# Optimization experiments

Hardware: AMD Instinct MI355X
Metric: run time of the kernel (lower is better)

The kernel has to match this reference:

```python
import jax, jax.numpy as jnp
import numpy as np

N_USERS, N_ITEMS = 3000, 3000
N = N_USERS + N_ITEMS
E = 100000
DIMS = [(N, 32), (32, 64), (64, 64), (64, 32)]  # RGCN layer (in,out) dims
NUM_REL = 2


def setup_inputs():
    key = jax.random.key(0)
    ks = iter(jax.random.split(key, 40))
    def p(shape, s=0.05):
        return jax.random.normal(next(ks), shape, dtype=jnp.float32) * s
    inp = {}
    for l, (i, o) in enumerate(DIMS):
        inp[f'basis{l}'] = p((4, i, o))      # basis matrices
        inp[f'comp{l}'] = p((NUM_REL, 4), 0.5)  # per-relation basis coefficients
        inp[f'root{l}'] = p((i, o))          # root/self weight
        inp[f'rbias{l}'] = jnp.zeros((o,), jnp.float32)
    inp['gat_w'] = p((32, 512))
    inp['gat_att_src'] = p((512,))
    inp['gat_att_dst'] = p((512,))
    inp['gat_bias'] = jnp.zeros((512,), jnp.float32)
    inp['w1'] = p((1024, 128))
    inp['b1'] = jnp.zeros((128,), jnp.float32)
    inp['w2'] = p((128, 1))
    inp['b2'] = jnp.zeros((1,), jnp.float32)
    inp['edge_index'] = jax.random.randint(next(ks), (2, E), 0, N)
    inp['edge_type'] = jax.random.randint(next(ks), (E,), 0, NUM_REL)
    return inp


def rgcn_layer(x, src, dst, edge_type, basis, comp, root, bias):
    # basis-decomposed relation weights: W[r] = sum_b comp[r,b] * basis[b]
    W = jnp.einsum('rb,bio->rio', comp, basis)  # [R, in, out]
    out = x @ root + bias                        # root/self term
    for r in range(NUM_REL):                     # fixed small relation count
        hr = x @ W[r]                            # [N, out]
        mask = (edge_type == r).astype(x.dtype)  # [E]
        msg = hr[src] * mask[:, None]            # gather + relation mask
        s = jax.ops.segment_sum(msg, dst, num_segments=N)
        cnt = jax.ops.segment_sum(mask, dst, num_segments=N)
        out = out + s / jnp.maximum(cnt, 1.0)[:, None]  # mean aggregation
    return out


def gat_layer(x, src, dst, w, a_src, a_dst, bias):
    # GATConv (1 head, negative_slope=0.2) with self-loops added (PyG default)
    loop = jnp.arange(N)
    s = jnp.concatenate([src, loop])
    d = jnp.concatenate([dst, loop])
    h = x @ w                      # [N, 512]
    asv = h @ a_src                # [N]
    adv = h @ a_dst                # [N]
    alpha = jax.nn.leaky_relu(asv[s] + adv[d], 0.2)  # [E+N]
    amax = jax.ops.segment_max(alpha, d, num_segments=N)
    amax = jnp.where(jnp.isneginf(amax), 0.0, amax)
    ex = jnp.exp(alpha - amax[d])
    denom = jax.ops.segment_sum(ex, d, num_segments=N)
    coef = ex / jnp.maximum(denom[d], 1e-16)
    out = jax.ops.segment_sum(h[s] * coef[:, None], d, num_segments=N)
    return out + bias


def reference(edge_index, edge_type,
              basis0, comp0, root0, rbias0,
              basis1, comp1, root1, rbias1,
              basis2, comp2, root2, rbias2,
              basis3, comp3, root3, rbias3,
              gat_w, gat_att_src, gat_att_dst, gat_bias,
              w1, b1, w2, b2):
    src, dst = edge_index[0], edge_index[1]
    convs = [(basis0, comp0, root0, rbias0), (basis1, comp1, root1, rbias1),
             (basis2, comp2, root2, rbias2), (basis3, comp3, root3, rbias3)]
    x = jnp.eye(N, dtype=jnp.float32)  # one-hot node features
    for (b, c, r, bi) in convs:
        x = jnp.tanh(rgcn_layer(x, src, dst, edge_type, b, c, r, bi))
    x = jax.nn.relu(gat_layer(x, src, dst, gat_w, gat_att_src, gat_att_dst, gat_bias))
    feat = jnp.concatenate([x[src], x[dst]], axis=1)  # [E, 1024]
    h = jax.nn.relu(feat @ w1 + b1)
    # F.dropout omitted (deterministic eval reference)
    out = jax.nn.sigmoid(h @ w2 + b2)
    return out.squeeze(-1)  # [E]
```

## Files before the change

### kernel.cpp

```cpp
#include <hip/hip_runtime.h>
#include <math.h>

#define NN 6000
#define EE 100000
#define ELL (EE + NN)
#define CAP 64

#define PK_SRC(p)  ((p) & 0x1FFF)
#define PK_REL(p)  (((p) >> 13) & 1)
#define PK_SELF(p) ((p) & 0x4000)

typedef __attribute__((ext_vector_type(8))) short frag8;
typedef __attribute__((ext_vector_type(4))) float f32x4;
typedef __attribute__((ext_vector_type(8))) unsigned short u16x8;

__device__ __forceinline__ unsigned short f2bf(float f){
  unsigned u = __float_as_uint(f);
  unsigned r = u + 0x7FFFu + ((u >> 16) & 1u);
  return (unsigned short)(r >> 16);
}
__device__ __forceinline__ float bf2f(unsigned short s){
  return __uint_as_float(((unsigned)s) << 16);
}

__global__ void k_pdc(const int* __restrict__ ei, const int* __restrict__ et,
                      int* __restrict__ cursor, int* __restrict__ pks,
                      const float* __restrict__ basis0, const float* __restrict__ comp0,
                      const float* __restrict__ b1,const float* __restrict__ c1,const float* __restrict__ r1,
                      const float* __restrict__ b2,const float* __restrict__ c2,const float* __restrict__ r2,
                      const float* __restrict__ b3,const float* __restrict__ c3,const float* __restrict__ r3,
                      const float* __restrict__ w1,
                      unsigned short* __restrict__ W016, float* __restrict__ Wcat,
                      unsigned short* __restrict__ Bt16){
  int t0 = blockIdx.x*256 + threadIdx.x;
  if (t0 < ELL){
    int d, pk;
    if (t0 < EE){
      d = ei[EE+t0];
      pk = ei[t0] | (et[t0] << 13);
    } else {
      d = t0 - EE; pk = d | 0x4000;
    }
    int pos = atomicAdd(&cursor[d], 1);
    pks[d*CAP + pos] = pk;
  }
  if (t0 < 2*NN*32){
    int r = t0 / (NN*32);
    int no = t0 - r*(NN*32);
    float acc = 0.f;
    #pragma unroll
    for (int b=0;b<4;b++) acc += comp0[r*4+b] * basis0[b*(NN*32)+no];
    W016[t0] = f2bf(acc);
    return;
  }
  int tw = t0 - 2*NN*32;
  if (tw < 24576){
    const float *bb,*cc,*rr; int I,O; int t = tw;
    if (tw < 6144)        { bb=b1;cc=c1;rr=r1;I=32;O=64; }
    else if (tw < 18432)  { bb=b2;cc=c2;rr=r2;I=64;O=64; t -= 6144; }
    else                  { bb=b3;cc=c3;rr=r3;I=64;O=32; t -= 18432; }
    int C = 3*O;
    int i = t / C; int col = t - i*C;
    float v;
    if (col < O) v = rr[i*O + col];
    else {
      int r = (col - O) / O; int o = col - O - r*O;
      v = 0.f;
      #pragma unroll
      for (int b=0;b<4;b++) v += cc[r*4+b]*bb[(b*I+i)*O + o];
    }
    Wcat[tw] = v;
    return;
  }
  int tb = tw - 24576;
  if (tb >= 256*512) return;
  int n = tb >> 9, k = tb & 511;
  float v = (n < 128) ? w1[k*128 + n] : w1[(512+k)*128 + (n-128)];
  Bt16[tb] = f2bf(v);
}

__global__ void __launch_bounds__(256) k_f1(
    const unsigned short* __restrict__ W016, const float* __restrict__ root,
    const float* __restrict__ rbias0,
    const int* __restrict__ degc, const int* __restrict__ pks,
    const float* __restrict__ Wc, unsigned short* __restrict__ Hout){
  __shared__ float sx[8*32];
  int n0 = blockIdx.x*8;
  int t = threadIdx.x, nl = t>>5, o = t&31, n = n0+nl;
  int r0 = n*CAP, deg = degc[n];
  int pk0 = (o      < deg) ? pks[r0 + o]      : 0x4000;
  int pk1 = (32 + o < deg) ? pks[r0 + 32 + o] : 0x4000;
  float a0 = 0.f, a1 = 0.f, c0 = 0.f, c1 = 0.f;
  int d0 = min(deg,32), d1 = deg - d0;
  for (int j=0;j<d0;j+=2){
    int pA = __shfl(pk0, j, 32);
    int pB = __shfl(pk0, j+1, 32);
    float vA = bf2f(W016[(PK_REL(pA)*NN + PK_SRC(pA))*32 + o]);
    float vB = bf2f(W016[(PK_REL(pB)*NN + PK_SRC(pB))*32 + o]);
    if (!PK_SELF(pA)){ if (PK_REL(pA)==0){ a0 += vA; c0 += 1.f; } else { a1 += vA; c1 += 1.f; } }
    if (!PK_SELF(pB)){ if (PK_REL(pB)==0){ a0 += vB; c0 += 1.f; } else { a1 += vB; c1 += 1.f; } }
  }
  for (int j=0;j<d1;j+=2){
    int pA = __shfl(pk1, j, 32);
    int pB = __shfl(pk1, j+1, 32);
    float vA = bf2f(W016[(PK_REL(pA)*NN + PK_SRC(pA))*32 + o]);
    float vB = bf2f(W016[(PK_REL(pB)*NN + PK_SRC(pB))*32 + o]);
    if (!PK_SELF(pA)){ if (PK_REL(pA)==0){ a0 += vA; c0 += 1.f; } else { a1 += vA; c1 += 1.f; } }
    if (!PK_SELF(pB)){ if (PK_REL(pB)==0){ a0 += vB; c0 += 1.f; } else { a1 += vB; c1 += 1.f; } }
  }
  sx[nl*32+o] = tanhf(root[n*32+o] + rbias0[o]
                      + a0/fmaxf(c0,1.f) + a1/fmaxf(c1,1.f));
  __syncthreads();
  if (t < 192){
    float acc[8] = {0,0,0,0,0,0,0,0};
    for (int i=0;i<32;i++){
      float w = Wc[i*192 + t];
      #pragma unroll
      for (int tt=0;tt<8;tt++) acc[tt] += sx[tt*32+i]*w;
    }
    #pragma unroll
    for (int tt=0;tt<8;tt++) Hout[(n0+tt)*192 + t] = f2bf(acc[tt]);
  }
}

__global__ void __launch_bounds__(256) k_f2(
    const unsigned short* __restrict__ Hin, const float* __restrict__ rbias,
    const int* __restrict__ degc, const int* __restrict__ pks,
    const float* __restrict__ Wc, unsigned short* __restrict__ Hout){
  __shared__ float sx[8*64];
  int n0 = blockIdx.x*8;
  int t = threadIdx.x, nl = t>>5, og = t&31, o0 = og*2, n = n0+nl;
  int r0 = n*CAP, deg = degc[n];
  int pk0 = (og      < deg) ? pks[r0 + og]      : 0x4000;
  int pk1 = (32 + og < deg) ? pks[r0 + 32 + og] : 0x4000;
  float a00=0.f, a01=0.f, a10=0.f, a11=0.f, c0=0.f, c1=0.f;
  int d0 = min(deg,32), d1 = deg - d0;
  for (int j=0;j<d0;j+=2){
    int pA = __shfl(pk0, j, 32);
    int pB = __shfl(pk0, j+1, 32);
    unsigned hvA = *(const unsigned*)&Hin[PK_SRC(pA)*192 + 64 + PK_REL(pA)*64 + o0];
    unsigned hvB = *(const unsigned*)&Hin[PK_SRC(pB)*192 + 64 + PK_REL(pB)*64 + o0];
    if (!PK_SELF(pA)){
      float v0 = bf2f((unsigned short)(hvA & 0xFFFF));
      float v1 = bf2f((unsigned short)(hvA >> 16));
      if (PK_REL(pA)==0){ a00 += v0; a01 += v1; c0 += 1.f; } else { a10 += v0; a11 += v1; c1 += 1.f; }
    }
    if (!PK_SELF(pB)){
      float v0 = bf2f((unsigned short)(hvB & 0xFFFF));
      float v1 = bf2f((unsigned short)(hvB >> 16));
      if (PK_REL(pB)==0){ a00 += v0; a01 += v1; c0 += 1.f; } else { a10 += v0; a11 += v1; c1 += 1.f; }
    }
  }
  for (int j=0;j<d1;j+=2){
    int pA = __shfl(pk1, j, 32);
    int pB = __shfl(pk1, j+1, 32);
    unsigned hvA = *(const unsigned*)&Hin[PK_SRC(pA)*192 + 64 + PK_REL(pA)*64 + o0];
    unsigned hvB = *(const unsigned*)&Hin[PK_SRC(pB)*192 + 64 + PK_REL(pB)*64 + o0];
    if (!PK_SELF(pA)){
      float v0 = bf2f((unsigned short)(hvA & 0xFFFF));
      float v1 = bf2f((unsigned short)(hvA >> 16));
      if (PK_REL(pA)==0){ a00 += v0; a01 += v1; c0 += 1.f; } else { a10 += v0; a11 += v1; c1 += 1.f; }
    }
    if (!PK_SELF(pB)){
      float v0 = bf2f((unsigned short)(hvB & 0xFFFF));
      float v1 = bf2f((unsigned short)(hvB >> 16));
      if (PK_REL(pB)==0){ a00 += v0; a01 += v1; c0 += 1.f; } else { a10 += v0; a11 += v1; c1 += 1.f; }
    }
  }
  float i0 = 1.f/fmaxf(c0,1.f), i1 = 1.f/fmaxf(c1,1.f);
  sx[nl*64+o0]   = tanhf(bf2f(Hin[n*192+o0])   + rbias[o0]   + a00*i0 + a10*i1);
  sx[nl*64+o0+1] = tanhf(bf2f(Hin[n*192+o0+1]) + rbias[o0+1] + a01*i0 + a11*i1);
  __syncthreads();
  if (t < 192){
    float acc[8] = {0,0,0,0,0,0,0,0};
    for (int i=0;i<64;i++){
      float w = Wc[i*192 + t];
      #pragma unroll
      for (int tt=0;tt<8;tt++) acc[tt] += sx[tt*64+i]*w;
    }
    #pragma unroll
    for (int tt=0;tt<8;tt++) Hout[(n0+tt)*192 + t] = f2bf(acc[tt]);
  }
}

__global__ void __launch_bounds__(256) k_f3(
    const unsigned short* __restrict__ Hin, const float* __restrict__ rbias,
    const int* __restrict__ degc, const int* __restrict__ pks,
    const float* __restrict__ Wc, unsigned short* __restrict__ Hout){
  __shared__ float sx[8*64];
  int n0 = blockIdx.x*8;
  int t = threadIdx.x, nl = t>>5, og = t&31, o0 = og*2, n = n0+nl;
  int r0 = n*CAP, deg = degc[n];
  int pk0 = (og      < deg) ? pks[r0 + og]      : 0x4000;
  int pk1 = (32 + og < deg) ? pks[r0 + 32 + og] : 0x4000;
  float a00=0.f, a01=0.f, a10=0.f, a11=0.f, c0=0.f, c1=0.f;
  int d0 = min(deg,32), d1 = deg - d0;
  for (int j=0;j<d0;j+=2){
    int pA = __shfl(pk0, j, 32);
    int pB = __shfl(pk0, j+1, 32);
    unsigned hvA = *(const unsigned*)&Hin[PK_SRC(pA)*192 + 64 + PK_REL(pA)*64 + o0];
    unsigned hvB = *(const unsigned*)&Hin[PK_SRC(pB)*192 + 64 + PK_REL(pB)*64 + o0];
    if (!PK_SELF(pA)){
      float v0 = bf2f((unsigned short)(hvA & 0xFFFF));
      float v1 = bf2f((unsigned short)(hvA >> 16));
      if (PK_REL(pA)==0){ a00 += v0; a01 += v1; c0 += 1.f; } else { a10 += v0; a11 += v1; c1 += 1.f; }
    }
    if (!PK_SELF(pB)){
      float v0 = bf2f((unsigned short)(hvB & 0xFFFF));
      float v1 = bf2f((unsigned short)(hvB >> 16));
      if (PK_REL(pB)==0){ a00 += v0; a01 += v1; c0 += 1.f; } else { a10 += v0; a11 += v1; c1 += 1.f; }
    }
  }
  for (int j=0;j<d1;j+=2){
    int pA = __shfl(pk1, j, 32);
    int pB = __shfl(pk1, j+1, 32);
    unsigned hvA = *(const unsigned*)&Hin[PK_SRC(pA)*192 + 64 + PK_REL(pA)*64 + o0];
    unsigned hvB = *(const unsigned*)&Hin[PK_SRC(pB)*192 + 64 + PK_REL(pB)*64 + o0];
    if (!PK_SELF(pA)){
      float v0 = bf2f((unsigned short)(hvA & 0xFFFF));
      float v1 = bf2f((unsigned short)(hvA >> 16));
      if (PK_REL(pA)==0){ a00 += v0; a01 += v1; c0 += 1.f; } else { a10 += v0; a11 += v1; c1 += 1.f; }
    }
    if (!PK_SELF(pB)){
      float v0 = bf2f((unsigned short)(hvB & 0xFFFF));
      float v1 = bf2f((unsigned short)(hvB >> 16));
      if (PK_REL(pB)==0){ a00 += v0; a01 += v1; c0 += 1.f; } else { a10 += v0; a11 += v1; c1 += 1.f; }
    }
  }
  float i0 = 1.f/fmaxf(c0,1.f), i1 = 1.f/fmaxf(c1,1.f);
  sx[nl*64+o0]   = tanhf(bf2f(Hin[n*192+o0])   + rbias[o0]   + a00*i0 + a10*i1);
  sx[nl*64+o0+1] = tanhf(bf2f(Hin[n*192+o0+1]) + rbias[o0+1] + a01*i0 + a11*i1);
  __syncthreads();
  if (t < 192){
    int c = t % 96, grp = t / 96;
    float acc[4] = {0,0,0,0};
    for (int i=0;i<64;i++){
      float w = Wc[i*96 + c];
      #pragma unroll
      for (int tt=0;tt<4;tt++) acc[tt] += sx[(grp*4+tt)*64+i]*w;
    }
    #pragma unroll
    for (int tt=0;tt<4;tt++) Hout[(n0+grp*4+tt)*96 + c] = f2bf(acc[tt]);
  }
}

__global__ void __launch_bounds__(256) k_f4(
    const unsigned short* __restrict__ Hin, const float* __restrict__ rbias,
    const int* __restrict__ degc, const int* __restrict__ pks,
    const float* __restrict__ gw, const float* __restrict__ as_,
    const float* __restrict__ ad_,
    unsigned short* __restrict__ h16, float* __restrict__ asv, float* __restrict__ adv){
  __shared__ float sx[8*32];
  __shared__ float red[4][16];
  int n0 = blockIdx.x*8;
  int t = threadIdx.x, nl = t>>5, o = t&31, n = n0+nl;
  int r0 = n*CAP, deg = degc[n];
  int pk0 = (o      < deg) ? pks[r0 + o]      : 0x4000;
  int pk1 = (32 + o < deg) ? pks[r0 + 32 + o] : 0x4000;
  float a0=0.f, a1=0.f, c0=0.f, c1=0.f;
  int d0 = min(deg,32), d1 = deg - d0;
  for (int j=0;j<d0;j+=2){
    int pA = __shfl(pk0, j, 32);
    int pB = __shfl(pk0, j+1, 32);
    float vA = bf2f(Hin[PK_SRC(pA)*96 + 32 + PK_REL(pA)*32 + o]);
    float vB = bf2f(Hin[PK_SRC(pB)*96 + 32 + PK_REL(pB)*32 + o]);
    if (!PK_SELF(pA)){ if (PK_REL(pA)==0){ a0 += vA; c0 += 1.f; } else { a1 += vA; c1 += 1.f; } }
    if (!PK_SELF(pB)){ if (PK_REL(pB)==0){ a0 += vB; c0 += 1.f; } else { a1 += vB; c1 += 1.f; } }
  }
  for (int j=0;j<d1;j+=2){
    int pA = __shfl(pk1, j, 32);
    int pB = __shfl(pk1, j+1, 32);
    float vA = bf2f(Hin[PK_SRC(pA)*96 + 32 + PK_REL(pA)*32 + o]);
    float vB = bf2f(Hin[PK_SRC(pB)*96 + 32 + PK_REL(pB)*32 + o]);
    if (!PK_SELF(pA)){ if (PK_REL(pA)==0){ a0 += vA; c0 += 1.f; } else { a1 += vA; c1 += 1.f; } }
    if (!PK_SELF(pB)){ if (PK_REL(pB)==0){ a0 += vB; c0 += 1.f; } else { a1 += vB; c1 += 1.f; } }
  }
  sx[nl*32+o] = tanhf(bf2f(Hin[n*96+o]) + rbias[o]
                      + a0/fmaxf(c0,1.f) + a1/fmaxf(c1,1.f));
  __syncthreads();
  int c2 = t*2;
  float2 acc[8];
  #pragma unroll
  for (int k=0;k<8;k++) acc[k] = {0.f,0.f};
  for (int i=0;i<32;i++){
    const float2 g = *(const float2*)&gw[i*512 + c2];
    #pragma unroll
    for (int k=0;k<8;k++){
      float xv = sx[k*32+i];
      acc[k].x += xv*g.x; acc[k].y += xv*g.y;
    }
  }
  const float2 a2 = *(const float2*)&as_[c2];
  const float2 d2 = *(const float2*)&ad_[c2];
  float sa[8], sd[8];
  #pragma unroll
  for (int k=0;k<8;k++){
    ushort2 ov;
    ov.x = f2bf(acc[k].x); ov.y = f2bf(acc[k].y);
    *(ushort2*)&h16[(n0+k)*512 + c2] = ov;
    sa[k] = acc[k].x*a2.x + acc[k].y*a2.y;
    sd[k] = acc[k].x*d2.x + acc[k].y*d2.y;
  }
  #pragma unroll
  for (int m=32;m>0;m>>=1){
    #pragma unroll
    for (int k=0;k<8;k++){ sa[k] += __shfl_xor(sa[k],m,64); sd[k] += __shfl_xor(sd[k],m,64); }
  }
  int wv = t>>6;
  if ((t&63)==0){
    #pragma unroll
    for (int k=0;k<8;k++){ red[wv][k]=sa[k]; red[wv][8+k]=sd[k]; }
  }
  __syncthreads();
  if (t<8)        asv[n0+t]   = red[0][t]+red[1][t]+red[2][t]+red[3][t];
  else if (t<16)  adv[n0+t-8] = red[0][t]+red[1][t]+red[2][t]+red[3][t];
}

__global__ void __launch_bounds__(64) k_gsa(
    const int* __restrict__ degc, const int* __restrict__ pks,
    const float* __restrict__ asv, const float* __restrict__ adv,
    const unsigned short* __restrict__ h16, const float* __restrict__ bias,
    unsigned short* __restrict__ gout16){
  int n = blockIdx.x;
  int lane = threadIdx.x;
  int r0 = n*CAP, deg = degc[n];
  float advn = adv[n];
  int pk  = (lane < deg) ? pks[r0 + lane] : -1;
  int src = (pk >= 0) ? PK_SRC(pk) : 0;
  float aa = -1e30f;
  if (pk >= 0){
    float a = asv[src] + advn;
    aa = (a >= 0.f) ? a : 0.2f*a;
  }
  float m = aa;
  #pragma unroll
  for (int off=32;off>0;off>>=1) m = fmaxf(m, __shfl_xor(m,off,64));
  float ex = (pk >= 0) ? expf(aa - m) : 0.f;
  float sumex = ex;
  #pragma unroll
  for (int off=32;off>0;off>>=1) sumex += __shfl_xor(sumex,off,64);
  float acc[8] = {0,0,0,0,0,0,0,0};
  for (int e=0;e<deg;e++){
    float cf = __shfl(ex, e, 64);
    int s    = __shfl(src, e, 64);
    const u16x8 hv = *(const u16x8*)&h16[(size_t)s*512 + lane*8];
    #pragma unroll
    for (int q=0;q<8;q++) acc[q] += cf * bf2f(hv[q]);
  }
  float inv = 1.f / fmaxf(sumex, 1e-16f);
  const float4 b0 = *(const float4*)&bias[lane*8];
  const float4 b1v = *(const float4*)&bias[lane*8+4];
  u16x8 o;
  o[0] = f2bf(fmaxf(acc[0]*inv + b0.x, 0.f));
  o[1] = f2bf(fmaxf(acc[1]*inv + b0.y, 0.f));
  o[2] = f2bf(fmaxf(acc[2]*inv + b0.z, 0.f));
  o[3] = f2bf(fmaxf(acc[3]*inv + b0.w, 0.f));
  o[4] = f2bf(fmaxf(acc[4]*inv + b1v.x, 0.f));
  o[5] = f2bf(fmaxf(acc[5]*inv + b1v.y, 0.f));
  o[6] = f2bf(fmaxf(acc[6]*inv + b1v.z, 0.f));
  o[7] = f2bf(fmaxf(acc[7]*inv + b1v.w, 0.f));
  *(u16x8*)&gout16[(size_t)n*512 + lane*8] = o;
}

__global__ void __launch_bounds__(64) k_AB(const unsigned short* __restrict__ gout16,
                                           const unsigned short* __restrict__ Bt16,
                                           unsigned short* __restrict__ P16){
  int lane = threadIdx.x;
  int mt = blockIdx.x >> 2;
  int nt = blockIdx.x & 3;
  int kq = (lane >> 4) * 8;
  const unsigned short* arow = gout16 + (size_t)(mt*16 + (lane & 15))*512 + kq;
  const unsigned short* bbase = Bt16 + (size_t)(nt*64 + (lane & 15))*512 + kq;
  f32x4 acc0 = {0,0,0,0}, acc1 = {0,0,0,0}, acc2 = {0,0,0,0}, acc3 = {0,0,0,0};
  for (int k = 0; k < 512; k += 32){
    frag8 a = *(const frag8*)(arow + k);
    frag8 b0 = *(const frag8*)(bbase + k);
    frag8 b1 = *(const frag8*)(bbase + 16*512 + k);
    frag8 b2 = *(const frag8*)(bbase + 32*512 + k);
    frag8 b3 = *(const frag8*)(bbase + 48*512 + k);
    acc0 = __builtin_amdgcn_mfma_f32_16x16x32_bf16(a, b0, acc0, 0, 0, 0);
    acc1 = __builtin_amdgcn_mfma_f32_16x16x32_bf16(a, b1, acc1, 0, 0, 0);
    acc2 = __builtin_amdgcn_mfma_f32_16x16x32_bf16(a, b2, acc2, 0, 0, 0);
    acc3 = __builtin_amdgcn_mfma_f32_16x16x32_bf16(a, b3, acc3, 0, 0, 0);
  }
  int rowb = mt*16 + (lane >> 4)*4;
  int col  = nt*64 + (lane & 15);
  #pragma unroll
  for (int i=0;i<4;i++){
    P16[(size_t)(rowb+i)*256 + col     ] = f2bf(acc0[i]);
    P16[(size_t)(rowb+i)*256 + col + 16] = f2bf(acc1[i]);
    P16[(size_t)(rowb+i)*256 + col + 32] = f2bf(acc2[i]);
    P16[(size_t)(rowb+i)*256 + col + 48] = f2bf(acc3[i]);
  }
}

__global__ void k_edge(const int* __restrict__ ei, const unsigned short* __restrict__ P16,
                       const float* __restrict__ b1,
                       const float* __restrict__ w2, const float* __restrict__ b2,
                       float* __restrict__ out){
  int e = blockIdx.x*16 + (threadIdx.x >> 4);
  int l = threadIdx.x & 15;
  if (e >= EE) return;
  int s = ei[e], d = ei[EE+e];
  const u16x8 Av = *(const u16x8*)&P16[(size_t)s*256 + l*8];
  const u16x8 Bv = *(const u16x8*)&P16[(size_t)d*256 + 128 + l*8];
  const float4 b1a = *(const float4*)&b1[l*8];
  const float4 b1b = *(const float4*)&b1[l*8+4];
  const float4 w2a = *(const float4*)&w2[l*8];
  const float4 w2b = *(const float4*)&w2[l*8+4];
  float h0 = fmaxf(bf2f(Av[0])+bf2f(Bv[0])+b1a.x, 0.f);
  float h1 = fmaxf(bf2f(Av[1])+bf2f(Bv[1])+b1a.y, 0.f);
  float h2 = fmaxf(bf2f(Av[2])+bf2f(Bv[2])+b1a.z, 0.f);
  float h3 = fmaxf(bf2f(Av[3])+bf2f(Bv[3])+b1a.w, 0.f);
  float h4 = fmaxf(bf2f(Av[4])+bf2f(Bv[4])+b1b.x, 0.f);
  float h5 = fmaxf(bf2f(Av[5])+bf2f(Bv[5])+b1b.y, 0.f);
  float h6 = fmaxf(bf2f(Av[6])+bf2f(Bv[6])+b1b.z, 0.f);
  float h7 = fmaxf(bf2f(Av[7])+bf2f(Bv[7])+b1b.w, 0.f);
  float acc = h0*w2a.x + h1*w2a.y + h2*w2a.z + h3*w2a.w
            + h4*w2b.x + h5*w2b.y + h6*w2b.z + h7*w2b.w;
  #pragma unroll
  for (int m=8;m>0;m>>=1) acc += __shfl_xor(acc,m,64);
  if (l==0) out[e] = 1.f/(1.f + expf(-(acc + b2[0])));
}

extern "C" void kernel_launch(void* const* d_in, const int* in_sizes, int n_in,
                              void* d_out, int out_size, void* d_ws, size_t ws_size,
                              hipStream_t stream){
  const float* basis0 = (const float*)d_in[0];
  const float* comp0  = (const float*)d_in[1];
  const float* root0  = (const float*)d_in[2];
  const float* rbias0 = (const float*)d_in[3];
  const float* basis1 = (const float*)d_in[4];
  const float* comp1  = (const float*)d_in[5];
  const float* root1  = (const float*)d_in[6];
  const float* rbias1 = (const float*)d_in[7];
  const float* basis2 = (const float*)d_in[8];
  const float* comp2  = (const float*)d_in[9];
  const float* root2  = (const float*)d_in[10];
  const float* rbias2 = (const float*)d_in[11];
  const float* basis3 = (const float*)d_in[12];
  const float* comp3  = (const float*)d_in[13];
  const float* root3  = (const float*)d_in[14];
  const float* rbias3 = (const float*)d_in[15];
  const float* gat_w = (const float*)d_in[16];
  const float* a_src = (const float*)d_in[17];
  const float* a_dst = (const float*)d_in[18];
  const float* gat_b = (const float*)d_in[19];
  const float* w1 = (const float*)d_in[20];
  const float* b1 = (const float*)d_in[21];
  const float* w2 = (const float*)d_in[22];
  const float* b2 = (const float*)d_in[23];
  const int* ei = (const int*)d_in[24];
  const int* et = (const int*)d_in[25];
  float* out = (float*)d_out;

  float* p = (float*)d_ws;
  int* cursor = (int*)p; p += NN;
  int* pks    = (int*)p; p += NN*CAP;
  unsigned short* W016 = (unsigned short*)p; p += NN*32;
  float* Wcat = p; p += 24576;
  unsigned short* Bt16 = (unsigned short*)p; p += 256*512/2;
  unsigned short* H16a = (unsigned short*)p; p += NN*96;
  unsigned short* H16b = (unsigned short*)p; p += NN*96;
  unsigned short* h16  = (unsigned short*)p; p += NN*256;
  float* asv  = p; p += NN;
  float* adv  = p; p += NN;
  unsigned short* gout16 = (unsigned short*)p; p += NN*256;
  unsigned short* P16 = (unsigned short*)p; p += NN*128;

  auto grid = [](long long n){ return dim3((unsigned)((n + 255)/256)); };

  hipMemsetAsync(cursor, 0, (size_t)NN*sizeof(int), stream);
  k_pdc<<<grid(2LL*NN*32 + 24576 + 256*512),256,0,stream>>>(ei, et, cursor, pks,
        basis0, comp0, basis1,comp1,root1, basis2,comp2,root2,
        basis3,comp3,root3, w1, W016, Wcat, Bt16);

  k_f1<<<dim3(NN/8),256,0,stream>>>(W016, root0, rbias0, cursor, pks, Wcat, H16a);
  k_f2<<<dim3(NN/8),256,0,stream>>>(H16a, rbias1, cursor, pks, Wcat + 6144, H16b);
  k_f3<<<dim3(NN/8),256,0,stream>>>(H16b, rbias2, cursor, pks, Wcat + 18432, H16a);
  k_f4<<<dim3(NN/8),256,0,stream>>>(H16a, rbias3, cursor, pks,
                                    gat_w, a_src, a_dst, h16, asv, adv);

  k_gsa<<<dim3(NN),64,0,stream>>>(cursor, pks, asv, adv, h16, gat_b, gout16);

  k_AB<<<dim3(1500),64,0,stream>>>(gout16, Bt16, P16);
  k_edge<<<dim3((EE+15)/16),256,0,stream>>>(ei, P16, b1, w2, b2, out);
}
```

Baseline: 204.8 us.

## Aggregate GAT over 32-dim inputs before projection and fuse with edge-MLP GEMM

Uses linearity of GAT aggregation: attention scores are computed from the 32-dim layer-4 output via the precomputed vectors gw·a_src and gw·a_dst. Neighbour aggregation now runs on 32-dim bf16 features instead of 512-dim projected rows, and the 512-wide projection is applied afterwards. The aggregation, projection with bias and ReLU, and the MFMA product with w1 are fused into one kernel held in shared memory. This removes the 512-wide h16 and gout16 buffers and two kernel launches. It adds a small serial reduction in setup and changes rounding because the projection is no longer quantised to bf16 before aggregation.

```diff
diff --git a/kernel.cpp b/kernel.cpp
--- a/kernel.cpp
+++ b/kernel.cpp
@@ -30,8 +30,10 @@
                       const float* __restrict__ b2,const float* __restrict__ c2,const float* __restrict__ r2,
                       const float* __restrict__ b3,const float* __restrict__ c3,const float* __restrict__ r3,
                       const float* __restrict__ w1,
+                      const float* __restrict__ gw, const float* __restrict__ a_src,
+                      const float* __restrict__ a_dst,
                       unsigned short* __restrict__ W016, float* __restrict__ Wcat,
-                      unsigned short* __restrict__ Bt16){
+                      unsigned short* __restrict__ Bt16, float* __restrict__ gwa){
   int t0 = blockIdx.x*256 + threadIdx.x;
   if (t0 < ELL){
     int d, pk;
@@ -73,10 +75,20 @@
     return;
   }
   int tb = tw - 24576;
-  if (tb >= 256*512) return;
-  int n = tb >> 9, k = tb & 511;
-  float v = (n < 128) ? w1[k*128 + n] : w1[(512+k)*128 + (n-128)];
-  Bt16[tb] = f2bf(v);
+  if (tb < 256*512){
+    int n = tb >> 9, k = tb & 511;
+    float v = (n < 128) ? w1[k*128 + n] : w1[(512+k)*128 + (n-128)];
+    Bt16[tb] = f2bf(v);
+    return;
+  }
+  int ti = tb - 256*512;
+  if (ti < 64){
+    const float* av = (ti < 32) ? a_src : a_dst;
+    int i = ti & 31;
+    float s = 0.f;
+    for (int k=0;k<512;k++) s += gw[i*512+k]*av[k];
+    gwa[ti] = s;
+  }
 }
 
 __global__ void __launch_bounds__(256) k_f1(
@@ -247,11 +259,8 @@
 __global__ void __launch_bounds__(256) k_f4(
     const unsigned short* __restrict__ Hin, const float* __restrict__ rbias,
     const int* __restrict__ degc, const int* __restrict__ pks,
-    const float* __restrict__ gw, const float* __restrict__ as_,
-    const float* __restrict__ ad_,
-    unsigned short* __restrict__ h16, float* __restrict__ asv, float* __restrict__ adv){
-  __shared__ float sx[8*32];
-  __shared__ float red[4][16];
+    const float* __restrict__ gwa,
+    unsigned short* __restrict__ X4, float* __restrict__ asv, float* __restrict__ adv){
   int n0 = blockIdx.x*8;
   int t = threadIdx.x, nl = t>>5, o = t&31, n = n0+nl;
   int r0 = n*CAP, deg = degc[n];
@@ -275,122 +284,107 @@
     if (!PK_SELF(pA)){ if (PK_REL(pA)==0){ a0 += vA; c0 += 1.f; } else { a1 += vA; c1 += 1.f; } }
     if (!PK_SELF(pB)){ if (PK_REL(pB)==0){ a0 += vB; c0 += 1.f; } else { a1 += vB; c1 += 1.f; } }
   }
-  sx[nl*32+o] = tanhf(bf2f(Hin[n*96+o]) + rbias[o]
-                      + a0/fmaxf(c0,1.f) + a1/fmaxf(c1,1.f));
-  __syncthreads();
-  int c2 = t*2;
-  float2 acc[8];
+  float v = tanhf(bf2f(Hin[n*96+o]) + rbias[o]
+                  + a0/fmaxf(c0,1.f) + a1/fmaxf(c1,1.f));
+  X4[n*32 + o] = f2bf(v);
+  float ss = v * gwa[o];
+  float sd = v * gwa[32+o];
   #pragma unroll
-  for (int k=0;k<8;k++) acc[k] = {0.f,0.f};
-  for (int i=0;i<32;i++){
-    const float2 g = *(const float2*)&gw[i*512 + c2];
-    #pragma unroll
-    for (int k=0;k<8;k++){
-      float xv = sx[k*32+i];
-      acc[k].x += xv*g.x; acc[k].y += xv*g.y;
-    }
-  }
-  const float2 a2 = *(const float2*)&as_[c2];
-  const float2 d2 = *(const float2*)&ad_[c2];
-  float sa[8], sd[8];
-  #pragma unroll
-  for (int k=0;k<8;k++){
-    ushort2 ov;
-    ov.x = f2bf(acc[k].x); ov.y = f2bf(acc[k].y);
-    *(ushort2*)&h16[(n0+k)*512 + c2] = ov;
-    sa[k] = acc[k].x*a2.x + acc[k].y*a2.y;
-    sd[k] = acc[k].x*d2.x + acc[k].y*d2.y;
-  }
-  #pragma unroll
-  for (int m=32;m>0;m>>=1){
-    #pragma unroll
-    for (int k=0;k<8;k++){ sa[k] += __shfl_xor(sa[k],m,64); sd[k] += __shfl_xor(sd[k],m,64); }
-  }
-  int wv = t>>6;
-  if ((t&63)==0){
-    #pragma unroll
-    for (int k=0;k<8;k++){ red[wv][k]=sa[k]; red[wv][8+k]=sd[k]; }
-  }
-  __syncthreads();
-  if (t<8)        asv[n0+t]   = red[0][t]+red[1][t]+red[2][t]+red[3][t];
-  else if (t<16)  adv[n0+t-8] = red[0][t]+red[1][t]+red[2][t]+red[3][t];
-}
-
-__global__ void __launch_bounds__(64) k_gsa(
+  for (int off=16;off>0;off>>=1){
+    ss += __shfl_xor(ss,off,64);
+    sd += __shfl_xor(sd,off,64);
+  }
+  if (o==0){ asv[n] = ss; adv[n] = sd; }
+}
+
+__global__ void __launch_bounds__(256) k_gpab(
     const int* __restrict__ degc, const int* __restrict__ pks,
     const float* __restrict__ asv, const float* __restrict__ adv,
-    const unsigned short* __restrict__ h16, const float* __restrict__ bias,
-    unsigned short* __restrict__ gout16){
-  int n = blockIdx.x;
-  int lane = threadIdx.x;
-  int r0 = n*CAP, deg = degc[n];
-  float advn = adv[n];
-  int pk  = (lane < deg) ? pks[r0 + lane] : -1;
-  int src = (pk >= 0) ? PK_SRC(pk) : 0;
-  float aa = -1e30f;
-  if (pk >= 0){
-    float a = asv[src] + advn;
-    aa = (a >= 0.f) ? a : 0.2f*a;
-  }
-  float m = aa;
-  #pragma unroll
-  for (int off=32;off>0;off>>=1) m = fmaxf(m, __shfl_xor(m,off,64));
-  float ex = (pk >= 0) ? expf(aa - m) : 0.f;
-  float sumex = ex;
-  #pragma unroll
-  for (int off=32;off>0;off>>=1) sumex += __shfl_xor(sumex,off,64);
-  float acc[8] = {0,0,0,0,0,0,0,0};
-  for (int e=0;e<deg;e++){
-    float cf = __shfl(ex, e, 64);
-    int s    = __shfl(src, e, 64);
-    const u16x8 hv = *(const u16x8*)&h16[(size_t)s*512 + lane*8];
-    #pragma unroll
-    for (int q=0;q<8;q++) acc[q] += cf * bf2f(hv[q]);
-  }
-  float inv = 1.f / fmaxf(sumex, 1e-16f);
-  const float4 b0 = *(const float4*)&bias[lane*8];
-  const float4 b1v = *(const float4*)&bias[lane*8+4];
-  u16x8 o;
-  o[0] = f2bf(fmaxf(acc[0]*inv + b0.x, 0.f));
-  o[1] = f2bf(fmaxf(acc[1]*inv + b0.y, 0.f));
-  o[2] = f2bf(fmaxf(acc[2]*inv + b0.z, 0.f));
-  o[3] = f2bf(fmaxf(acc[3]*inv + b0.w, 0.f));
-  o[4] = f2bf(fmaxf(acc[4]*inv + b1v.x, 0.f));
-  o[5] = f2bf(fmaxf(acc[5]*inv + b1v.y, 0.f));
-  o[6] = f2bf(fmaxf(acc[6]*inv + b1v.z, 0.f));
-  o[7] = f2bf(fmaxf(acc[7]*inv + b1v.w, 0.f));
-  *(u16x8*)&gout16[(size_t)n*512 + lane*8] = o;
-}
-
-__global__ void __launch_bounds__(64) k_AB(const unsigned short* __restrict__ gout16,
-                                           const unsigned short* __restrict__ Bt16,
-                                           unsigned short* __restrict__ P16){
-  int lane = threadIdx.x;
-  int mt = blockIdx.x >> 2;
-  int nt = blockIdx.x & 3;
-  int kq = (lane >> 4) * 8;
-  const unsigned short* arow = gout16 + (size_t)(mt*16 + (lane & 15))*512 + kq;
-  const unsigned short* bbase = Bt16 + (size_t)(nt*64 + (lane & 15))*512 + kq;
-  f32x4 acc0 = {0,0,0,0}, acc1 = {0,0,0,0}, acc2 = {0,0,0,0}, acc3 = {0,0,0,0};
-  for (int k = 0; k < 512; k += 32){
-    frag8 a = *(const frag8*)(arow + k);
-    frag8 b0 = *(const frag8*)(bbase + k);
-    frag8 b1 = *(const frag8*)(bbase + 16*512 + k);
-    frag8 b2 = *(const frag8*)(bbase + 32*512 + k);
-    frag8 b3 = *(const frag8*)(bbase + 48*512 + k);
-    acc0 = __builtin_amdgcn_mfma_f32_16x16x32_bf16(a, b0, acc0, 0, 0, 0);
-    acc1 = __builtin_amdgcn_mfma_f32_16x16x32_bf16(a, b1, acc1, 0, 0, 0);
-    acc2 = __builtin_amdgcn_mfma_f32_16x16x32_bf16(a, b2, acc2, 0, 0, 0);
-    acc3 = __builtin_amdgcn_mfma_f32_16x16x32_bf16(a, b3, acc3, 0, 0, 0);
-  }
-  int rowb = mt*16 + (lane >> 4)*4;
-  int col  = nt*64 + (lane & 15);
-  #pragma unroll
-  for (int i=0;i<4;i++){
-    P16[(size_t)(rowb+i)*256 + col     ] = f2bf(acc0[i]);
-    P16[(size_t)(rowb+i)*256 + col + 16] = f2bf(acc1[i]);
-    P16[(size_t)(rowb+i)*256 + col + 32] = f2bf(acc2[i]);
-    P16[(size_t)(rowb+i)*256 + col + 48] = f2bf(acc3[i]);
+    const unsigned short* __restrict__ X4, const float* __restrict__ gw,
+    const float* __restrict__ gat_b, const unsigned short* __restrict__ Bt16,
+    unsigned short* __restrict__ P16){
+  __shared__ float xa[16][33];
+  __shared__ unsigned short go[16*520];
+  int t = threadIdx.x, w = t>>6, lane = t&63;
+  int n0 = blockIdx.x*16;
+  for (int s=0;s<4;s++){
+    int nl = w*4 + s, n = n0 + nl;
+    int r0 = n*CAP, deg = degc[n];
+    float advn = adv[n];
+    int pk  = (lane < deg) ? pks[r0 + lane] : -1;
+    int src = (pk >= 0) ? PK_SRC(pk) : 0;
+    float aa = -1e30f;
+    if (pk >= 0){
+      float a = asv[src] + advn;
+      aa = (a >= 0.f) ? a : 0.2f*a;
+    }
+    float m = aa;
+    #pragma unroll
+    for (int off=32;off>0;off>>=1) m = fmaxf(m, __shfl_xor(m,off,64));
+    float ex = (pk >= 0) ? expf(aa - m) : 0.f;
+    float se = ex;
+    #pragma unroll
+    for (int off=32;off>0;off>>=1) se += __shfl_xor(se,off,64);
+    float inv = 1.f / fmaxf(se, 1e-16f);
+    int c = lane & 31, hh = lane >> 5;
+    float acc = 0.f;
+    for (int e=0;e<deg;e+=2){
+      float cf = __shfl(ex, e+hh, 64);
+      int   sv = __shfl(src, e+hh, 64);
+      acc += cf * bf2f(X4[sv*32 + c]);
+    }
+    acc += __shfl_xor(acc, 32, 64);
+    if (hh == 0) xa[nl][c] = acc * inv;
+  }
+  __syncthreads();
+  {
+    int c2 = t*2;
+    float2 acc2[16];
+    #pragma unroll
+    for (int k=0;k<16;k++) acc2[k] = {0.f,0.f};
+    for (int i=0;i<32;i++){
+      const float2 g = *(const float2*)&gw[i*512 + c2];
+      #pragma unroll
+      for (int k=0;k<16;k++){
+        float xv = xa[k][i];
+        acc2[k].x += xv*g.x; acc2[k].y += xv*g.y;
+      }
+    }
+    const float2 bv = *(const float2*)&gat_b[c2];
+    #pragma unroll
+    for (int k=0;k<16;k++){
+      ushort2 ov;
+      ov.x = f2bf(fmaxf(acc2[k].x + bv.x, 0.f));
+      ov.y = f2bf(fmaxf(acc2[k].y + bv.y, 0.f));
+      *(ushort2*)&go[k*520 + c2] = ov;
+    }
+  }
+  __syncthreads();
+  {
+    int kq = (lane >> 4) * 8;
+    const unsigned short* arow  = go + (lane & 15)*520 + kq;
+    const unsigned short* bbase = Bt16 + (size_t)(w*64 + (lane & 15))*512 + kq;
+    f32x4 acc0 = {0,0,0,0}, acc1 = {0,0,0,0}, acc2 = {0,0,0,0}, acc3 = {0,0,0,0};
+    for (int k = 0; k < 512; k += 32){
+      frag8 a  = *(const frag8*)(arow + k);
+      frag8 b0 = *(const frag8*)(bbase + k);
+      frag8 b1 = *(const frag8*)(bbase + 16*512 + k);
+      frag8 b2 = *(const frag8*)(bbase + 32*512 + k);
+      frag8 b3 = *(const frag8*)(bbase + 48*512 + k);
+      acc0 = __builtin_amdgcn_mfma_f32_16x16x32_bf16(a, b0, acc0, 0, 0, 0);
+      acc1 = __builtin_amdgcn_mfma_f32_16x16x32_bf16(a, b1, acc1, 0, 0, 0);
+      acc2 = __builtin_amdgcn_mfma_f32_16x16x32_bf16(a, b2, acc2, 0, 0, 0);
+      acc3 = __builtin_amdgcn_mfma_f32_16x16x32_bf16(a, b3, acc3, 0, 0, 0);
+    }
+    int rowb = n0 + (lane >> 4)*4;
+    int col  = w*64 + (lane & 15);
+    #pragma unroll
+    for (int i=0;i<4;i++){
+      P16[(size_t)(rowb+i)*256 + col     ] = f2bf(acc0[i]);
+      P16[(size_t)(rowb+i)*256 + col + 16] = f2bf(acc1[i]);
+      P16[(size_t)(rowb+i)*256 + col + 32] = f2bf(acc2[i]);
+      P16[(size_t)(rowb+i)*256 + col + 48] = f2bf(acc3[i]);
+    }
   }
 }
 
@@ -462,27 +456,26 @@
   unsigned short* Bt16 = (unsigned short*)p; p += 256*512/2;
   unsigned short* H16a = (unsigned short*)p; p += NN*96;
   unsigned short* H16b = (unsigned short*)p; p += NN*96;
-  unsigned short* h16  = (unsigned short*)p; p += NN*256;
+  unsigned short* X4   = (unsigned short*)p; p += NN*16;
+  float* gwa  = p; p += 64;
   float* asv  = p; p += NN;
   float* adv  = p; p += NN;
-  unsigned short* gout16 = (unsigned short*)p; p += NN*256;
   unsigned short* P16 = (unsigned short*)p; p += NN*128;
 
   auto grid = [](long long n){ return dim3((unsigned)((n + 255)/256)); };
 
   hipMemsetAsync(cursor, 0, (size_t)NN*sizeof(int), stream);
-  k_pdc<<<grid(2LL*NN*32 + 24576 + 256*512),256,0,stream>>>(ei, et, cursor, pks,
+  k_pdc<<<grid(2LL*NN*32 + 24576 + 256*512 + 64),256,0,stream>>>(ei, et, cursor, pks,
         basis0, comp0, basis1,comp1,root1, basis2,comp2,root2,
-        basis3,comp3,root3, w1, W016, Wcat, Bt16);
+        basis3,comp3,root3, w1, gat_w, a_src, a_dst, W016, Wcat, Bt16, gwa);
 
   k_f1<<<dim3(NN/8),256,0,stream>>>(W016, root0, rbias0, cursor, pks, Wcat, H16a);
   k_f2<<<dim3(NN/8),256,0,stream>>>(H16a, rbias1, cursor, pks, Wcat + 6144, H16b);
   k_f3<<<dim3(NN/8),256,0,stream>>>(H16b, rbias2, cursor, pks, Wcat + 18432, H16a);
-  k_f4<<<dim3(NN/8),256,0,stream>>>(H16a, rbias3, cursor, pks,
-                                    gat_w, a_src, a_dst, h16, asv, adv);
-
-  k_gsa<<<dim3(NN),64,0,stream>>>(cursor, pks, asv, adv, h16, gat_b, gout16);
-
-  k_AB<<<dim3(1500),64,0,stream>>>(gout16, Bt16, P16);
+  k_f4<<<dim3(NN/8),256,0,stream>>>(H16a, rbias3, cursor, pks, gwa, X4, asv, adv);
+
+  k_gpab<<<dim3(NN/16),256,0,stream>>>(cursor, pks, asv, adv, X4, gat_w, gat_b,
+                                       Bt16, P16);
+
   k_edge<<<dim3((EE+15)/16),256,0,stream>>>(ei, P16, b1, w2, b2, out);
 }
```

Result: slower. 209.1 us (+2.1%).
